# Kernel tuning notes

Measured on AMD Instinct MI355X. Metric: run time of the kernel, lower is better.

The kernel has to match this reference:

```python
import jax, jax.numpy as jnp
import numpy as np

GROUPS = 6  # attn_group in Stack

def setup_inputs() -> dict:
    key = jax.random.key(0)
    k0, k1, k2, k3, k4 = jax.random.split(key, 5)
    B, S, IN, OUT, K = 2, 2048, 512, 768, 31
    fan = (2.0 / IN) ** 0.5  # kaiming_normal fan_out-ish scale
    x = jax.random.normal(k0, (B, S, IN), jnp.float32)
    W_q = jax.random.normal(k1, (OUT, IN), jnp.float32) * fan
    W_k = jax.random.normal(k2, (OUT, IN), jnp.float32) * fan
    W_v = jax.random.normal(k3, (OUT, IN), jnp.float32) * fan
    rel = jax.random.normal(k4, (OUT, K), jnp.float32)
    return {"x": x, "W_q": W_q, "W_k": W_k, "W_v": W_v, "rel": rel}

def reference(x, W_q, W_k, W_v, rel):
    B, S, _ = x.shape
    OUT, K = rel.shape
    pad = (K - 1) // 2
    d = OUT // GROUPS
    # projections
    q = x @ W_q.T                                   # [B,S,OUT]
    xp = jnp.pad(x, ((0, 0), (pad, pad), (0, 0)))    # pad seq dim
    k = xp @ W_k.T                                  # [B,S+K-1,OUT]
    v = xp @ W_v.T
    # unfold: window of size K per query position (stride 1)
    idx = jnp.arange(S)[:, None] + jnp.arange(K)[None, :]   # [S,K]
    k_win = k[:, idx, :] + rel.T                    # [B,S,K,OUT], rel bias (out,K)->(K,out)
    v_win = v[:, idx, :]                            # [B,S,K,OUT]
    k_win = k_win.reshape(B, S, K, GROUPS, d)
    v_win = v_win.reshape(B, S, K, GROUPS, d)
    qg = q.reshape(B, S, GROUPS, d)
    energy = jnp.einsum('bsgd,bskgd->bsgk', qg, k_win)       # QK dot over head dim
    attn = jax.nn.softmax(energy, axis=-1)                   # softmax over window
    out = jnp.einsum('bsgk,bskgd->bsgd', attn, v_win).reshape(B, S, OUT)
    return out, attn  # attn matches torch attention.squeeze(3): [B,S,groups,K]
```

## Files before the change

kernel.cpp:

```cpp
#include <hip/hip_runtime.h>
#include <hip/hip_bf16.h>

#define S_LEN 2048
#define B_SZ 2
#define IN_DIM 512
#define OUT_DIM 768
#define KWIN 31
#define PAD 15
#define NGROUP 6
#define DHEAD 128
#define M_TOT 4096
#define N_TOT 2304
#define QK_W 1536

typedef __attribute__((ext_vector_type(8))) __bf16 bf16x8;
typedef __attribute__((ext_vector_type(8))) unsigned short u16x8;
typedef __attribute__((ext_vector_type(4))) float f32x4;

static __device__ __forceinline__ unsigned short f2bf(float f) {
  unsigned int u = __float_as_uint(f);
  unsigned int r = (u + 0x7fffu + ((u >> 16) & 1u)) >> 16;
  return (unsigned short)r;
}
static __device__ __forceinline__ float bf2f(unsigned short h) {
  return __uint_as_float(((unsigned int)h) << 16);
}

__global__ __launch_bounds__(256) void prep_kernel(
    const float* __restrict__ x,
    const float* __restrict__ Wq, const float* __restrict__ Wk, const float* __restrict__ Wv,
    const float* __restrict__ rel,
    unsigned short* __restrict__ xhi, unsigned short* __restrict__ xlo,
    unsigned short* __restrict__ whi, unsigned short* __restrict__ wlo,
    unsigned short* __restrict__ relThi, unsigned short* __restrict__ relTlo,
    unsigned short* __restrict__ zpage) {
  const int bid = blockIdx.x;
  const int tid = threadIdx.x;
  if (bid < 2048) {
    int i = bid * 256 + tid;
    float4 v = ((const float4*)x)[i];
    unsigned short h0 = f2bf(v.x), h1 = f2bf(v.y), h2 = f2bf(v.z), h3 = f2bf(v.w);
    ((ushort4*)xhi)[i] = make_ushort4(h0, h1, h2, h3);
    ((ushort4*)xlo)[i] = make_ushort4(f2bf(v.x - bf2f(h0)), f2bf(v.y - bf2f(h1)),
                                      f2bf(v.z - bf2f(h2)), f2bf(v.w - bf2f(h3)));
  } else if (bid < 3200) {
    int i = (bid - 2048) * 256 + tid;
    int e = i * 4;
    const int per = OUT_DIM * IN_DIM;
    const float* src = (e < per) ? Wq : (e < 2 * per) ? Wk : Wv;
    int rem = (e < per) ? e : (e < 2 * per) ? e - per : e - 2 * per;
    float4 v = *(const float4*)(src + rem);
    unsigned short h0 = f2bf(v.x), h1 = f2bf(v.y), h2 = f2bf(v.z), h3 = f2bf(v.w);
    ((ushort4*)whi)[i] = make_ushort4(h0, h1, h2, h3);
    ((ushort4*)wlo)[i] = make_ushort4(f2bf(v.x - bf2f(h0)), f2bf(v.y - bf2f(h1)),
                                      f2bf(v.z - bf2f(h2)), f2bf(v.w - bf2f(h3)));
  } else if (bid < 3293) {
    int idx = (bid - 3200) * 256 + tid;
    int kk = idx / OUT_DIM;
    int o = idx - kk * OUT_DIM;
    float v = rel[o * KWIN + kk];
    unsigned short h = f2bf(v);
    relThi[idx] = h;
    relTlo[idx] = f2bf(v - bf2f(h));
  } else {
    if (tid < 128) zpage[tid] = 0;
  }
}

#define SLOTB 49152

static __device__ __forceinline__ int swz32(int O) {
  return O ^ (((O >> 7) & 3) << 4);
}

#define MFMA16(AF, BF) \
  _Pragma("unroll") for (int mi = 0; mi < 4; ++mi) \
  _Pragma("unroll") for (int ni = 0; ni < 4; ++ni) \
    acc[mi][ni] = __builtin_amdgcn_mfma_f32_16x16x32_bf16( \
        AF[mi], BF[ni], acc[mi][ni], 0, 0, 0);

#define READ_AHI() _Pragma("unroll") for (int mi = 0; mi < 4; ++mi) ahi[mi] = *(const bf16x8*)(slot + aoff[mi]);
#define READ_ALO() _Pragma("unroll") for (int mi = 0; mi < 4; ++mi) alo[mi] = *(const bf16x8*)(slot + 16384 + aoff[mi]);
#define READ_WHI() _Pragma("unroll") for (int ni = 0; ni < 4; ++ni) whi[ni] = *(const bf16x8*)(slot + 32768 + boff[ni]);
#define READ_WLO() _Pragma("unroll") for (int ni = 0; ni < 4; ++ni) wlo[ni] = *(const bf16x8*)(slot + 40960 + boff[ni]);

#define END_BARRIER() \
  __builtin_amdgcn_s_barrier(); \
  asm volatile("" ::: "memory");

__global__ __launch_bounds__(512, 2) void gemm_kernel(
    const unsigned short* __restrict__ Ahi, const unsigned short* __restrict__ Alo,
    const unsigned short* __restrict__ Whi, const unsigned short* __restrict__ Wlo,
    unsigned short* __restrict__ qkhi, unsigned short* __restrict__ qklo,
    unsigned short* __restrict__ vTw) {
  __shared__ unsigned short lds_u16[73728];
  char* ldsb = (char*)lds_u16;
  const int tid = threadIdx.x;
  const int wid = tid >> 6, lane = tid & 63;
  const int elr = lane & 15, elq = lane >> 4;
  const int wm = wid >> 1, wn = wid & 1;

  int aoff[4], boff[4];
#pragma unroll
  for (int mi = 0; mi < 4; ++mi)
    aoff[mi] = swz32((wm * 64 + mi * 16 + elr) * 64 + elq * 16);
#pragma unroll
  for (int ni = 0; ni < 4; ++ni)
    boff[ni] = swz32((wn * 64 + ni * 16 + elr) * 64 + elq * 16);

  const int strow = tid >> 2;
  const int stcol = (((tid & 3) ^ ((tid >> 3) & 3)) << 3);

  auto stage8k = [&](char* slot, int RO, int j, const unsigned short* src,
                     int grow0, int kloc) {
    const unsigned short* g = src + (size_t)(grow0 + j * 128 + strow) * IN_DIM + kloc + stcol;
    __builtin_amdgcn_global_load_lds((const __attribute__((address_space(1))) void*)g,
        (__attribute__((address_space(3))) void*)(slot + RO + j * 8192 + wid * 1024), 16, 0, 0);
  };

  f32x4 acc[4][4] = {};
  bf16x8 ahi[4], whi[4], alo[4], wlo[4];

  const int bid = blockIdx.x;

  if (bid < 192) {
    const int bm = bid & 15, ct = bid >> 4;
    const int row0 = bm << 8, col0 = ct << 7;

    auto stageChunk = [&](int cc) {
      char* s = ldsb + (cc % 3) * SLOTB;
      const int pk = cc << 5;
      stage8k(s, 0, 0, Ahi, row0, pk);      stage8k(s, 0, 1, Ahi, row0, pk);
      stage8k(s, 16384, 0, Alo, row0, pk);  stage8k(s, 16384, 1, Alo, row0, pk);
      stage8k(s, 32768, 0, Whi, col0, pk);  stage8k(s, 40960, 0, Wlo, col0, pk);
    };

    stageChunk(0);
    stageChunk(1);
    asm volatile("s_waitcnt vmcnt(6)" ::: "memory");
    END_BARRIER()

    for (int c = 0; c < 16; ++c) {
      char* slot = ldsb + (c % 3) * SLOTB;
      READ_AHI()
      READ_WHI()
      READ_ALO()
      READ_WLO()
      const bool pref = (c + 2) < 16;
      if (pref) stageChunk(c + 2);
      __builtin_amdgcn_s_setprio(1);
      MFMA16(ahi, whi)
      MFMA16(alo, whi)
      MFMA16(ahi, wlo)
      __builtin_amdgcn_s_setprio(0);
      if (pref) { asm volatile("s_waitcnt vmcnt(6)" ::: "memory"); }
      else      { asm volatile("s_waitcnt vmcnt(0)" ::: "memory"); }
      END_BARRIER()
    }

    const int elg = elq * 4;
#pragma unroll
    for (int mi = 0; mi < 4; ++mi)
#pragma unroll
      for (int ni = 0; ni < 4; ++ni) {
        int ncol = col0 + wn * 64 + ni * 16 + elr;
        size_t rbase = (size_t)(row0 + wm * 64 + mi * 16 + elg);
#pragma unroll
        for (int j = 0; j < 4; ++j) {
          float v = acc[mi][ni][j];
          unsigned short h = f2bf(v);
          size_t idx = (rbase + j) * QK_W + ncol;
          qkhi[idx] = h;
          qklo[idx] = f2bf(v - bf2f(h));
        }
      }
  } else {
    const int bid2 = bid - 192;
    const int bm = bid2 & 15, grp = bid2 >> 4;
    const int row0 = bm << 8;
    auto vcol = [&](int ci) { return 1536 + ((grp * 2 + (ci >> 4)) << 7); };

    auto stageChunkV = [&](int cc) {
      char* s = ldsb + (cc % 3) * SLOTB;
      const int pk = (cc & 15) << 5;
      stage8k(s, 0, 0, Ahi, row0, pk);  stage8k(s, 0, 1, Ahi, row0, pk);
      stage8k(s, 32768, 0, Whi, vcol(cc), pk);
    };

    stageChunkV(0);
    stageChunkV(1);
    asm volatile("s_waitcnt vmcnt(3)" ::: "memory");
    END_BARRIER()

    for (int ci = 0; ci < 32; ++ci) {
      char* slot = ldsb + (ci % 3) * SLOTB;
      READ_AHI()
      READ_WHI()
      const bool pref = (ci + 2) < 32;
      if (pref) stageChunkV(ci + 2);
      __builtin_amdgcn_s_setprio(1);
      MFMA16(ahi, whi)
      __builtin_amdgcn_s_setprio(0);
      if (pref) { asm volatile("s_waitcnt vmcnt(3)" ::: "memory"); }
      else      { asm volatile("s_waitcnt vmcnt(0)" ::: "memory"); }
      END_BARRIER()

      if ((ci & 15) == 15) {
        const int col0 = vcol(ci);
        const int elg = elq * 4;
#pragma unroll
        for (int mi = 0; mi < 4; ++mi)
#pragma unroll
          for (int ni = 0; ni < 4; ++ni) {
            int d = col0 - 1536 + wn * 64 + ni * 16 + elr;
            int srw = row0 + wm * 64 + mi * 16 + elg;
            ushort4 pk4;
            pk4.x = f2bf(acc[mi][ni][0]); pk4.y = f2bf(acc[mi][ni][1]);
            pk4.z = f2bf(acc[mi][ni][2]); pk4.w = f2bf(acc[mi][ni][3]);
            *(ushort4*)(vTw + (size_t)d * M_TOT + srw) = pk4;
            acc[mi][ni] = (f32x4){0.f, 0.f, 0.f, 0.f};
          }
      }
    }
  }
}

__global__ __launch_bounds__(256, 3) void attn_kernel(
    const unsigned short* __restrict__ qkhi, const unsigned short* __restrict__ qklo,
    const unsigned short* __restrict__ vT,
    const unsigned short* __restrict__ relThi, const unsigned short* __restrict__ relTlo,
    const unsigned short* __restrict__ zpage,
    float* __restrict__ out, float* __restrict__ attn_out) {
  __shared__ __attribute__((aligned(16))) unsigned short smem[22528];
  char* smb = (char*)smem;
  float* Elds = (float*)(smb + 24576);
  const int VT_BASE = 24576;
  const int AB_BASE = 40960;

  const int tid = threadIdx.x;
  const int wid = tid >> 6, lane = tid & 63;
  const int bid = (blockIdx.x & 7) * 96 + (blockIdx.x >> 3);
  const int tile = bid & 63;
  const int g = (bid >> 6) % NGROUP;
  const int b = bid / (64 * NGROUP);
  const int s0 = tile * 32;
  const size_t rowbase = (size_t)b * S_LEN;
  const int elr = lane & 15, elq = lane >> 4;

  {
    const int wrow = wid * 4 + (lane >> 4);
    const int kcb = lane & 15;
#pragma unroll
    for (int i = 0; i < 6; ++i) {
      int w = i * 16 + wrow;
      int scb = (kcb ^ (w & 7)) * 8;
      const unsigned short* gp;
      if (w < 62) {
        int r = s0 - 15 + w;
        gp = (r >= 0 && r < S_LEN)
           ? qkhi + (size_t)(rowbase + r) * QK_W + OUT_DIM + g * DHEAD + scb
           : zpage + scb;
      } else if (w < 93) {
        gp = relThi + (w - 62) * OUT_DIM + g * DHEAD + scb;
      } else {
        gp = zpage + scb;
      }
      __builtin_amdgcn_global_load_lds((const __attribute__((address_space(1))) void*)gp,
          (__attribute__((address_space(3))) void*)(smb + (i * 16 + wid * 4) * 256 + (lane & 15) * 16 + (lane >> 4) * 256),
          16, 0, 0);
    }
  }
  {
    int O = tid * 16;
    O ^= (O >> 3) & 0x70;
    u16x8 z = {};
    *(u16x8*)(smb + AB_BASE + O) = z;
  }

  const int rf = wid & 1;
  const int cb3 = 3 * (wid >> 1);
  bf16x8 qh[4], ql[4];
  {
    size_t qrow = rowbase + s0 + rf * 16 + elr;
    const unsigned short* qb  = qkhi + qrow * QK_W + g * DHEAD + elq * 8;
    const unsigned short* qb2 = qklo + qrow * QK_W + g * DHEAD + elq * 8;
#pragma unroll
    for (int ks = 0; ks < 4; ++ks) {
      qh[ks] = *(const bf16x8*)(qb + ks * 32);
      ql[ks] = *(const bf16x8*)(qb2 + ks * 32);
    }
  }
  __syncthreads();

#pragma unroll
  for (int cf = 0; cf < 3; ++cf) {
    int c = cb3 + cf;
    const unsigned short* klbase;
    {
      int w = c * 16 + elr;
      int r = s0 - 15 + w;
      if (w < 62)      klbase = (r >= 0 && r < S_LEN)
                                ? qklo + (size_t)(rowbase + r) * QK_W + OUT_DIM + g * DHEAD
                                : zpage;
      else if (w < 93) klbase = relTlo + (w - 62) * OUT_DIM + g * DHEAD;
      else             klbase = zpage;
    }
    bf16x8 kl[4];
#pragma unroll
    for (int ks = 0; ks < 4; ++ks)
      kl[ks] = *(const bf16x8*)(klbase + ks * 32 + elq * 8);

    f32x4 ea = {};
#pragma unroll
    for (int ks = 0; ks < 4; ++ks) {
      int O = (c * 16 + elr) * 256 + ks * 64 + elq * 16;
      int Os = O ^ ((O >> 4) & 0x70);
      bf16x8 kh = *(const bf16x8*)(smb + Os);
      __builtin_amdgcn_s_setprio(1);
      ea = __builtin_amdgcn_mfma_f32_16x16x32_bf16(qh[ks], kh, ea, 0, 0, 0);
      ea = __builtin_amdgcn_mfma_f32_16x16x32_bf16(ql[ks], kh, ea, 0, 0, 0);
      ea = __builtin_amdgcn_mfma_f32_16x16x32_bf16(qh[ks], kl[ks], ea, 0, 0, 0);
      __builtin_amdgcn_s_setprio(0);
    }
#pragma unroll
    for (int j = 0; j < 4; ++j)
      Elds[(rf * 16 + elq * 4 + j) * 96 + c * 16 + elr] = ea[j];
  }
  __syncthreads();

  {
    const int kkl = lane & 31;
    const int half = lane >> 5;
    const int kkc = (kkl < 31) ? kkl : 30;
#pragma unroll
    for (int p = 0; p < 4; ++p) {
      int si = p * 8 + wid * 2 + half;
      float e = Elds[si * 96 + si + kkc] + Elds[si * 96 + 62 + kkc];
      if (kkl == 31) e = -INFINITY;
      float m = e;
#pragma unroll
      for (int off = 16; off > 0; off >>= 1) m = fmaxf(m, __shfl_xor(m, off, 32));
      float pr = __expf(e - m);
      float sum = pr;
#pragma unroll
      for (int off = 16; off > 0; off >>= 1) sum += __shfl_xor(sum, off, 32);
      float a = pr / sum;
      if (kkl < 31) {
        attn_out[((rowbase + s0 + si) * NGROUP + g) * KWIN + kkl] = a;
        int O = si * 128 + (si + kkl + 1) * 2;
        O ^= (O >> 3) & 0x70;
        *(unsigned short*)(smb + AB_BASE + O) = f2bf(a);
      }
    }
  }
  __syncthreads();

  {
    const unsigned short* vsrc = vT + (size_t)g * DHEAD * M_TOT + (size_t)b * S_LEN;
    const int drow = wid * 8 + (lane >> 3);
    const int vcb = lane & 7;
#pragma unroll
    for (int i = 0; i < 4; ++i) {
      int d = i * 32 + drow;
      int sl = s0 - 16 + (vcb ^ (d & 7)) * 8;
      const unsigned short* gp = (sl >= 0 && sl < S_LEN)
        ? vsrc + (size_t)d * M_TOT + sl
        : zpage + (vcb ^ (d & 7)) * 8;
      __builtin_amdgcn_global_load_lds((const __attribute__((address_space(1))) void*)gp,
          (__attribute__((address_space(3))) void*)(smb + VT_BASE + (i * 32 + wid * 8) * 128 + (lane >> 3) * 128 + (lane & 7) * 16),
          16, 0, 0);
    }
  }
  __syncthreads();

  {
    const int pcb = 4 * (wid >> 1);
    f32x4 pa[4] = {};
#pragma unroll
    for (int ks = 0; ks < 2; ++ks) {
      int AO = (rf * 16 + elr) * 128 + ks * 64 + elq * 16;
      AO ^= (AO >> 3) & 0x70;
      bf16x8 afr = *(const bf16x8*)(smb + AB_BASE + AO);
      __builtin_amdgcn_s_setprio(1);
#pragma unroll
      for (int cf = 0; cf < 4; ++cf) {
        int VO = ((pcb + cf) * 16 + elr) * 128 + ks * 64 + elq * 16;
        VO ^= (VO >> 3) & 0x70;
        bf16x8 vfr = *(const bf16x8*)(smb + VT_BASE + VO);
        pa[cf] = __builtin_amdgcn_mfma_f32_16x16x32_bf16(afr, vfr, pa[cf], 0, 0, 0);
      }
      __builtin_amdgcn_s_setprio(0);
    }
#pragma unroll
    for (int cf = 0; cf < 4; ++cf)
#pragma unroll
      for (int j = 0; j < 4; ++j)
        out[(rowbase + s0 + rf * 16 + elq * 4 + j) * OUT_DIM + g * DHEAD + pcb * 16 + cf * 16 + elr]
            = pa[cf][j];
  }
}

extern "C" void kernel_launch(void* const* d_in, const int* in_sizes, int n_in,
                              void* d_out, int out_size, void* d_ws, size_t ws_size,
                              hipStream_t stream) {
  const float* x   = (const float*)d_in[0];
  const float* Wq  = (const float*)d_in[1];
  const float* Wk  = (const float*)d_in[2];
  const float* Wv  = (const float*)d_in[3];
  const float* rel = (const float*)d_in[4];

  char* ws = (char*)d_ws;
  unsigned short* Ahi    = (unsigned short*)(ws);
  unsigned short* Alo    = (unsigned short*)(ws + 4194304);
  unsigned short* Whi    = (unsigned short*)(ws + 8388608);
  unsigned short* Wlo    = (unsigned short*)(ws + 10747904);
  unsigned short* relThi = (unsigned short*)(ws + 13107200);
  unsigned short* relTlo = (unsigned short*)(ws + 13154816);
  unsigned short* qkhi   = (unsigned short*)(ws + 13202432);
  unsigned short* qklo   = (unsigned short*)(ws + 25785344);
  unsigned short* vTw    = (unsigned short*)(ws + 38368256);
  unsigned short* zpage  = (unsigned short*)(ws + 44659712);

  float* outp = (float*)d_out;
  float* attn = outp + (size_t)B_SZ * S_LEN * OUT_DIM;

  prep_kernel<<<3294, 256, 0, stream>>>(x, Wq, Wk, Wv, rel, Ahi, Alo, Whi, Wlo,
                                        relThi, relTlo, zpage);
  gemm_kernel<<<240, 512, 0, stream>>>(Ahi, Alo, Whi, Wlo, qkhi, qklo, vTw);
  attn_kernel<<<768, 256, 0, stream>>>(qkhi, qklo, vTw, relThi, relTlo, zpage, outp, attn);
}
```

Baseline: 53.45 us.

## Fuse x bf16 hi/lo split into GEMM LDS read path

Removes the prep-kernel pass that split x into bf16 hi and lo arrays. The GEMM now stages fp32 x straight into LDS with a new swizzle and converts each fragment to hi/lo bf16 in registers with packed convert instructions. This drops a full write-and-reread of x through global memory and shrinks the prep launch. In exchange, every GEMM block redoes the conversion on each LDS read, which adds VALU work to the MFMA loop. The V path now also stages fp32 A it did not need as lo, doubling its A traffic.

```diff
diff --git a/kernel.cpp b/kernel.cpp
--- a/kernel.cpp
+++ b/kernel.cpp
@@ -16,6 +16,7 @@
 typedef __attribute__((ext_vector_type(8))) __bf16 bf16x8;
 typedef __attribute__((ext_vector_type(8))) unsigned short u16x8;
 typedef __attribute__((ext_vector_type(4))) float f32x4;
+typedef __attribute__((ext_vector_type(4))) unsigned int u32x4;
 
 static __device__ __forceinline__ unsigned short f2bf(float f) {
   unsigned int u = __float_as_uint(f);
@@ -26,25 +27,35 @@
   return __uint_as_float(((unsigned int)h) << 16);
 }
 
+static __device__ __forceinline__ void cvt_split8(f32x4 a0, f32x4 a1,
+                                                  bf16x8* hi, bf16x8* lo) {
+  unsigned int h[4], l[4];
+#define PAIR(idx, fA, fB)                                                      \
+  {                                                                            \
+    asm("v_cvt_pk_bf16_f32 %0, %1, %2" : "=v"(h[idx]) : "v"(fA), "v"(fB));     \
+    float r0 = (fA) - __uint_as_float(h[idx] << 16);                           \
+    float r1 = (fB) - __uint_as_float(h[idx] & 0xffff0000u);                   \
+    asm("v_cvt_pk_bf16_f32 %0, %1, %2" : "=v"(l[idx]) : "v"(r0), "v"(r1));     \
+  }
+  PAIR(0, a0[0], a0[1]) PAIR(1, a0[2], a0[3])
+  PAIR(2, a1[0], a1[1]) PAIR(3, a1[2], a1[3])
+#undef PAIR
+  u32x4 hv = {h[0], h[1], h[2], h[3]};
+  u32x4 lv = {l[0], l[1], l[2], l[3]};
+  *hi = __builtin_bit_cast(bf16x8, hv);
+  *lo = __builtin_bit_cast(bf16x8, lv);
+}
+
 __global__ __launch_bounds__(256) void prep_kernel(
-    const float* __restrict__ x,
     const float* __restrict__ Wq, const float* __restrict__ Wk, const float* __restrict__ Wv,
     const float* __restrict__ rel,
-    unsigned short* __restrict__ xhi, unsigned short* __restrict__ xlo,
     unsigned short* __restrict__ whi, unsigned short* __restrict__ wlo,
     unsigned short* __restrict__ relThi, unsigned short* __restrict__ relTlo,
     unsigned short* __restrict__ zpage) {
   const int bid = blockIdx.x;
   const int tid = threadIdx.x;
-  if (bid < 2048) {
+  if (bid < 1152) {
     int i = bid * 256 + tid;
-    float4 v = ((const float4*)x)[i];
-    unsigned short h0 = f2bf(v.x), h1 = f2bf(v.y), h2 = f2bf(v.z), h3 = f2bf(v.w);
-    ((ushort4*)xhi)[i] = make_ushort4(h0, h1, h2, h3);
-    ((ushort4*)xlo)[i] = make_ushort4(f2bf(v.x - bf2f(h0)), f2bf(v.y - bf2f(h1)),
-                                      f2bf(v.z - bf2f(h2)), f2bf(v.w - bf2f(h3)));
-  } else if (bid < 3200) {
-    int i = (bid - 2048) * 256 + tid;
     int e = i * 4;
     const int per = OUT_DIM * IN_DIM;
     const float* src = (e < per) ? Wq : (e < 2 * per) ? Wk : Wv;
@@ -54,8 +65,8 @@
     ((ushort4*)whi)[i] = make_ushort4(h0, h1, h2, h3);
     ((ushort4*)wlo)[i] = make_ushort4(f2bf(v.x - bf2f(h0)), f2bf(v.y - bf2f(h1)),
                                       f2bf(v.z - bf2f(h2)), f2bf(v.w - bf2f(h3)));
-  } else if (bid < 3293) {
-    int idx = (bid - 3200) * 256 + tid;
+  } else if (bid < 1245) {
+    int idx = (bid - 1152) * 256 + tid;
     int kk = idx / OUT_DIM;
     int o = idx - kk * OUT_DIM;
     float v = rel[o * KWIN + kk];
@@ -79,8 +90,12 @@
     acc[mi][ni] = __builtin_amdgcn_mfma_f32_16x16x32_bf16( \
         AF[mi], BF[ni], acc[mi][ni], 0, 0, 0);
 
-#define READ_AHI() _Pragma("unroll") for (int mi = 0; mi < 4; ++mi) ahi[mi] = *(const bf16x8*)(slot + aoff[mi]);
-#define READ_ALO() _Pragma("unroll") for (int mi = 0; mi < 4; ++mi) alo[mi] = *(const bf16x8*)(slot + 16384 + aoff[mi]);
+#define READ_AX() \
+  _Pragma("unroll") for (int mi = 0; mi < 4; ++mi) { \
+    f32x4 a0 = *(const f32x4*)(slot + axoff[mi][0]); \
+    f32x4 a1 = *(const f32x4*)(slot + axoff[mi][1]); \
+    cvt_split8(a0, a1, &ahi[mi], &alo[mi]); \
+  }
 #define READ_WHI() _Pragma("unroll") for (int ni = 0; ni < 4; ++ni) whi[ni] = *(const bf16x8*)(slot + 32768 + boff[ni]);
 #define READ_WLO() _Pragma("unroll") for (int ni = 0; ni < 4; ++ni) wlo[ni] = *(const bf16x8*)(slot + 40960 + boff[ni]);
 
@@ -89,7 +104,7 @@
   asm volatile("" ::: "memory");
 
 __global__ __launch_bounds__(512, 2) void gemm_kernel(
-    const unsigned short* __restrict__ Ahi, const unsigned short* __restrict__ Alo,
+    const float* __restrict__ xf,
     const unsigned short* __restrict__ Whi, const unsigned short* __restrict__ Wlo,
     unsigned short* __restrict__ qkhi, unsigned short* __restrict__ qklo,
     unsigned short* __restrict__ vTw) {
@@ -100,22 +115,34 @@
   const int elr = lane & 15, elq = lane >> 4;
   const int wm = wid >> 1, wn = wid & 1;
 
-  int aoff[4], boff[4];
-#pragma unroll
-  for (int mi = 0; mi < 4; ++mi)
-    aoff[mi] = swz32((wm * 64 + mi * 16 + elr) * 64 + elq * 16);
+  int axoff[4][2];
+#pragma unroll
+  for (int mi = 0; mi < 4; ++mi) {
+    int rrow = mi * 16 + elr;
+    int O1 = rrow * 128 + elq * 32;
+    int sw = (rrow & 7) << 4;
+    axoff[mi][0] = wm * 8192 + (O1 ^ sw);
+    axoff[mi][1] = wm * 8192 + ((O1 + 16) ^ sw);
+  }
+  int boff[4];
 #pragma unroll
   for (int ni = 0; ni < 4; ++ni)
     boff[ni] = swz32((wn * 64 + ni * 16 + elr) * 64 + elq * 16);
 
+  const int xrow = tid >> 3;
+  const int xcol = (((tid & 7) ^ ((tid >> 3) & 7)) << 2);
   const int strow = tid >> 2;
   const int stcol = (((tid & 3) ^ ((tid >> 3) & 3)) << 3);
 
-  auto stage8k = [&](char* slot, int RO, int j, const unsigned short* src,
-                     int grow0, int kloc) {
-    const unsigned short* g = src + (size_t)(grow0 + j * 128 + strow) * IN_DIM + kloc + stcol;
+  auto stageX = [&](char* slot, int j, int row0, int kloc) {
+    const float* g = xf + (size_t)(row0 + j * 64 + xrow) * IN_DIM + kloc + xcol;
     __builtin_amdgcn_global_load_lds((const __attribute__((address_space(1))) void*)g,
-        (__attribute__((address_space(3))) void*)(slot + RO + j * 8192 + wid * 1024), 16, 0, 0);
+        (__attribute__((address_space(3))) void*)(slot + j * 8192 + wid * 1024), 16, 0, 0);
+  };
+  auto stageW = [&](char* slot, int RO, const unsigned short* src, int gcol0, int kloc) {
+    const unsigned short* g = src + (size_t)(gcol0 + strow) * IN_DIM + kloc + stcol;
+    __builtin_amdgcn_global_load_lds((const __attribute__((address_space(1))) void*)g,
+        (__attribute__((address_space(3))) void*)(slot + RO + wid * 1024), 16, 0, 0);
   };
 
   f32x4 acc[4][4] = {};
@@ -130,9 +157,10 @@
     auto stageChunk = [&](int cc) {
       char* s = ldsb + (cc % 3) * SLOTB;
       const int pk = cc << 5;
-      stage8k(s, 0, 0, Ahi, row0, pk);      stage8k(s, 0, 1, Ahi, row0, pk);
-      stage8k(s, 16384, 0, Alo, row0, pk);  stage8k(s, 16384, 1, Alo, row0, pk);
-      stage8k(s, 32768, 0, Whi, col0, pk);  stage8k(s, 40960, 0, Wlo, col0, pk);
+      stageX(s, 0, row0, pk); stageX(s, 1, row0, pk);
+      stageX(s, 2, row0, pk); stageX(s, 3, row0, pk);
+      stageW(s, 32768, Whi, col0, pk);
+      stageW(s, 40960, Wlo, col0, pk);
     };
 
     stageChunk(0);
@@ -142,9 +170,8 @@
 
     for (int c = 0; c < 16; ++c) {
       char* slot = ldsb + (c % 3) * SLOTB;
-      READ_AHI()
+      READ_AX()
       READ_WHI()
-      READ_ALO()
       READ_WLO()
       const bool pref = (c + 2) < 16;
       if (pref) stageChunk(c + 2);
@@ -183,25 +210,26 @@
     auto stageChunkV = [&](int cc) {
       char* s = ldsb + (cc % 3) * SLOTB;
       const int pk = (cc & 15) << 5;
-      stage8k(s, 0, 0, Ahi, row0, pk);  stage8k(s, 0, 1, Ahi, row0, pk);
-      stage8k(s, 32768, 0, Whi, vcol(cc), pk);
+      stageX(s, 0, row0, pk); stageX(s, 1, row0, pk);
+      stageX(s, 2, row0, pk); stageX(s, 3, row0, pk);
+      stageW(s, 32768, Whi, vcol(cc), pk);
     };
 
     stageChunkV(0);
     stageChunkV(1);
-    asm volatile("s_waitcnt vmcnt(3)" ::: "memory");
+    asm volatile("s_waitcnt vmcnt(5)" ::: "memory");
     END_BARRIER()
 
     for (int ci = 0; ci < 32; ++ci) {
       char* slot = ldsb + (ci % 3) * SLOTB;
-      READ_AHI()
+      READ_AX()
       READ_WHI()
       const bool pref = (ci + 2) < 32;
       if (pref) stageChunkV(ci + 2);
       __builtin_amdgcn_s_setprio(1);
       MFMA16(ahi, whi)
       __builtin_amdgcn_s_setprio(0);
-      if (pref) { asm volatile("s_waitcnt vmcnt(3)" ::: "memory"); }
+      if (pref) { asm volatile("s_waitcnt vmcnt(5)" ::: "memory"); }
       else      { asm volatile("s_waitcnt vmcnt(0)" ::: "memory"); }
       END_BARRIER()
 
@@ -410,8 +438,6 @@
   const float* rel = (const float*)d_in[4];
 
   char* ws = (char*)d_ws;
-  unsigned short* Ahi    = (unsigned short*)(ws);
-  unsigned short* Alo    = (unsigned short*)(ws + 4194304);
   unsigned short* Whi    = (unsigned short*)(ws + 8388608);
   unsigned short* Wlo    = (unsigned short*)(ws + 10747904);
   unsigned short* relThi = (unsigned short*)(ws + 13107200);
@@ -424,8 +450,7 @@
   float* outp = (float*)d_out;
   float* attn = outp + (size_t)B_SZ * S_LEN * OUT_DIM;
 
-  prep_kernel<<<3294, 256, 0, stream>>>(x, Wq, Wk, Wv, rel, Ahi, Alo, Whi, Wlo,
-                                        relThi, relTlo, zpage);
-  gemm_kernel<<<240, 512, 0, stream>>>(Ahi, Alo, Whi, Wlo, qkhi, qklo, vTw);
+  prep_kernel<<<1246, 256, 0, stream>>>(Wq, Wk, Wv, rel, Whi, Wlo, relThi, relTlo, zpage);
+  gemm_kernel<<<240, 512, 0, stream>>>(x, Whi, Wlo, qkhi, qklo, vTw);
   attn_kernel<<<768, 256, 0, stream>>>(qkhi, qklo, vTw, relThi, relTlo, zpage, outp, attn);
 }
```

New measurement: 59.25 us. +10.9%, slower.
